# Optimization experiments

Hardware: AMD Instinct MI355X
Metric: run time of the kernel (lower is better)

## Reference

```python
import jax, jax.numpy as jnp
import numpy as np

BITS = 4
GROUP = 128
PACK = 32 // BITS  # 8 values per int32
MASK = (1 << BITS) - 1


def _unpack_weight(qweight, K, N):
    # qweight: [K//PACK, N] int32; PACK 4-bit values packed along K in each int32
    shifts = jnp.arange(PACK, dtype=jnp.int32) * BITS  # [PACK]
    w = (qweight[:, None, :] >> shifts[None, :, None]) & MASK  # [K//PACK, PACK, N]
    return w.reshape(K, N)


def _unpack_zeros(qzeros, G, N):
    # qzeros: [G, N//PACK] int32; PACK 4-bit values packed along N in each int32
    shifts = jnp.arange(PACK, dtype=jnp.int32) * BITS  # [PACK]
    z = (qzeros[:, :, None] >> shifts[None, None, :]) & MASK  # [G, N//PACK, PACK]
    return z.reshape(G, N)


def setup_inputs() -> dict:
    key = jax.random.key(0)
    k1, k2, k3, k4 = jax.random.split(key, 4)
    B, S, K, N = 4, 1024, 4096, 11008
    G = K // GROUP
    x = jax.random.normal(k1, (B, S, K), dtype=jnp.float32)
    qweight = jax.random.randint(k2, (K // PACK, N), 0, 2147483647, dtype=jnp.int32)
    qzeros = jax.random.randint(k3, (G, N // PACK), 0, 2147483647, dtype=jnp.int32)
    scales = jax.random.uniform(k4, (G, N), dtype=jnp.float32) * 0.01
    return {"x": x, "qweight": qweight, "qzeros": qzeros, "scales": scales}


def reference(x, qweight, qzeros, scales):
    K = x.shape[-1]
    G, N = scales.shape
    # dequantize: W[k, n] = (q[k, n] - zero[g(k), n]) * scale[g(k), n]
    w_q = _unpack_weight(qweight, K, N).astype(jnp.float32)   # [K, N]
    zeros = _unpack_zeros(qzeros, G, N).astype(jnp.float32)   # [G, N]
    gid = jnp.arange(K) // GROUP                              # [K]
    W = (w_q - zeros[gid]) * scales[gid]                      # [K, N]
    return jnp.einsum('bsk,kn->bsn', x, W)
```

## Files before the change

### kernel.cpp

```cpp
#include <hip/hip_runtime.h>


#define BK 32
#define LDK 40
#define TILE_BYTES 10240

typedef _Float16 v8h __attribute__((ext_vector_type(8)));
typedef _Float16 half2v __attribute__((ext_vector_type(2)));
typedef float v4f __attribute__((ext_vector_type(4)));

__device__ __forceinline__ unsigned pkrtz_u32(float a, float b) {
  return __builtin_bit_cast(unsigned, __builtin_amdgcn_cvt_pkrtz(a, b));
}

__device__ __forceinline__ void load_lds_16B(const void* g, void* l) {
  __builtin_amdgcn_global_load_lds(
      (const __attribute__((address_space(1))) unsigned*)g,
      (__attribute__((address_space(3))) unsigned*)l, 16, 0, 0);
}

__global__ __launch_bounds__(256)
void prep_x(const float* __restrict__ x, unsigned short* __restrict__ xt, int K) {
  const int kt = blockIdx.x, mt = blockIdx.y;
  const int t = threadIdx.x;
  const int row = t >> 1, half = t & 1;
  const float* src = x + (size_t)(mt * 128 + row) * K + kt * 32 + half * 16;
  const float4 v0 = ((const float4*)src)[0];
  const float4 v1 = ((const float4*)src)[1];
  const float4 v2 = ((const float4*)src)[2];
  const float4 v3 = ((const float4*)src)[3];
  uint4 o0, o1;
  o0.x = pkrtz_u32(v0.x, v0.y); o0.y = pkrtz_u32(v0.z, v0.w);
  o0.z = pkrtz_u32(v1.x, v1.y); o0.w = pkrtz_u32(v1.z, v1.w);
  o1.x = pkrtz_u32(v2.x, v2.y); o1.y = pkrtz_u32(v2.z, v2.w);
  o1.z = pkrtz_u32(v3.x, v3.y); o1.w = pkrtz_u32(v3.z, v3.w);
  unsigned short* dst =
      xt + (size_t)(mt * (K / 32) + kt) * (TILE_BYTES / 2) + row * LDK + half * 16;
  ((uint4*)dst)[0] = o0;
  ((uint4*)(dst + 8))[0] = o1;
}

__global__ __launch_bounds__(512, 4)
void qgemm_dma(const unsigned short* __restrict__ xt,
               const unsigned* __restrict__ qweight,
               const unsigned* __restrict__ qzeros,
               const float* __restrict__ scales,
               float* __restrict__ out,
               int M, int N, int K) {
  __shared__ __align__(16) short As[128][LDK];
  __shared__ __align__(16) short Bs[256][LDK];

  const int tid = threadIdx.x;
  const int lane = tid & 63;
  const int wid = tid >> 6;
  const int n0 = blockIdx.x * 256;
  const int m0 = blockIdx.y * 128;
  const int mt = blockIdx.y;
  const int wm = (wid >> 2) * 64;
  const int wn = (wid & 3) * 64;
  const int lr = lane & 15;
  const int lk = (lane >> 4) * 8;

  const int b_n = tid & 255;
  const int b_kr0 = tid >> 8;
  const int gn = n0 + b_n;
  const unsigned* qwb = qweight + (size_t)b_kr0 * N + gn;

  const char* xt_b = (const char*)xt;
  const int NT = K / BK;

  v4f acc[4][4] = {};

  unsigned b0c, b1c, zpc;
  float scc;
  auto load_b = [&](int t, unsigned& b0, unsigned& b1, unsigned& zp, float& sc) {
    const int kk = t * BK;
    const size_t qoff = (size_t)(kk >> 3) * N;
    b0 = qwb[qoff];
    b1 = qwb[qoff + 2 * (size_t)N];
    const int g = kk >> 7;
    zp = qzeros[(size_t)g * (N >> 3) + (gn >> 3)];
    sc = scales[(size_t)g * N + gn];
  };
  load_b(0, b0c, b1c, zpc, scc);

#pragma unroll 2
  for (int t = 0; t < NT; ++t) {
    {
      const char* g = xt_b + (size_t)(mt * NT + t) * TILE_BYTES +
                      (size_t)wid * 1024 + (size_t)lane * 16;
      char* l = ((char*)&As[0][0]) + wid * 1024;
      load_lds_16B(g, l);
      if (wid < 2) load_lds_16B(g + 8 * 1024, l + 8 * 1024);
    }

    {
      const unsigned z = (zpc >> ((gn & 7) * 4)) & 15u;
      const unsigned hz_u = 0x64006400u | z | (z << 16);
      const half2v hz2 = __builtin_bit_cast(half2v, hz_u);
      const half2v hs2 = __builtin_bit_cast(half2v, pkrtz_u32(scc, scc));
      const unsigned qvs[2] = {b0c, b1c};
#pragma unroll
      for (int q = 0; q < 2; ++q) {
        const int kr = b_kr0 + q * 2;
        const unsigned qv = qvs[q];
        uint4 wv;
        unsigned* wp = (unsigned*)&wv;
#pragma unroll
        for (int j = 0; j < 4; ++j) {
          const unsigned byte = qv >> (8 * j);
          const unsigned pq = 0x64006400u | (byte & 0xFu) | ((byte & 0xF0u) << 12);
          const half2v w2 = (__builtin_bit_cast(half2v, pq) - hz2) * hs2;
          wp[j] = __builtin_bit_cast(unsigned, w2);
        }
        *(uint4*)(&Bs[b_n][kr * 8]) = wv;
      }
    }

    __syncthreads();

    unsigned b0n, b1n, zpn;
    float scn;
    const int tn = (t + 1 < NT) ? (t + 1) : t;
    load_b(tn, b0n, b1n, zpn, scn);

    v8h af[4], bfr[4];
#pragma unroll
    for (int i = 0; i < 4; ++i) {
      af[i] = *(const v8h*)(&As[wm + i * 16 + lr][lk]);
      bfr[i] = *(const v8h*)(&Bs[wn + i * 16 + lr][lk]);
    }
#pragma unroll
    for (int mi = 0; mi < 4; ++mi) {
#pragma unroll
      for (int ni = 0; ni < 4; ++ni) {
        acc[mi][ni] = __builtin_amdgcn_mfma_f32_16x16x32_f16(
            af[mi], bfr[ni], acc[mi][ni], 0, 0, 0);
      }
    }

    __syncthreads();

    b0c = b0n; b1c = b1n; zpc = zpn; scc = scn;
  }

#pragma unroll
  for (int mi = 0; mi < 4; ++mi) {
#pragma unroll
    for (int ni = 0; ni < 4; ++ni) {
#pragma unroll
      for (int r = 0; r < 4; ++r) {
        const int row = m0 + wm + mi * 16 + (lane >> 4) * 4 + r;
        const int col = n0 + wn + ni * 16 + lr;
        out[(size_t)row * N + col] = acc[mi][ni][r];
      }
    }
  }
}

__global__ __launch_bounds__(256, 2)
void qgemm_fused(const float* __restrict__ x,
                 const unsigned* __restrict__ qweight,
                 const unsigned* __restrict__ qzeros,
                 const float* __restrict__ scales,
                 float* __restrict__ out,
                 int M, int N, int K) {
  __shared__ short As[128][LDK];
  __shared__ short Bs[128][LDK];

  const int tid = threadIdx.x;
  const int lane = tid & 63;
  const int wid = tid >> 6;
  const int n0 = blockIdx.x * 128;
  const int m0 = blockIdx.y * 128;
  const int wm = (wid >> 1) * 64;
  const int wn = (wid & 1) * 64;
  const int lr = lane & 15;
  const int lk = (lane >> 4) * 8;

  const int a_row = tid >> 3;
  const int a_col = (tid & 7) * 4;
  const int b_n = tid & 127;
  const int b_kr0 = tid >> 7;
  const int gn = n0 + b_n;

  const float* xb = x + (size_t)(m0 + a_row) * K + a_col;
  const unsigned* qwb = qweight + (size_t)b_kr0 * N + gn;

  v4f acc[4][4] = {};
  const int NT = K / BK;

  float4 axc[4];
  unsigned b0c, b1c, zpc;
  float scc;

  auto load_step = [&](int t, float4 ax[4], unsigned& b0, unsigned& b1,
                       unsigned& zp, float& sc) {
    const int kk = t * BK;
#pragma unroll
    for (int p = 0; p < 4; ++p)
      ax[p] = *(const float4*)(xb + (size_t)(p * 32) * K + kk);
    const size_t qoff = (size_t)(kk >> 3) * N;
    b0 = qwb[qoff];
    b1 = qwb[qoff + 2 * (size_t)N];
    const int g = kk >> 7;
    zp = qzeros[(size_t)g * (N >> 3) + (gn >> 3)];
    sc = scales[(size_t)g * N + gn];
  };

  load_step(0, axc, b0c, b1c, zpc, scc);

#pragma unroll 2
  for (int t = 0; t < NT; ++t) {
    const unsigned z = (zpc >> ((gn & 7) * 4)) & 15u;
    const unsigned hz_u = 0x64006400u | z | (z << 16);
    const half2v hz2 = __builtin_bit_cast(half2v, hz_u);
    const half2v hs2 = __builtin_bit_cast(half2v, pkrtz_u32(scc, scc));

#pragma unroll
    for (int p = 0; p < 4; ++p) {
      const int row = p * 32 + a_row;
      uint2 pv;
      pv.x = pkrtz_u32(axc[p].x, axc[p].y);
      pv.y = pkrtz_u32(axc[p].z, axc[p].w);
      *(uint2*)(&As[row][a_col]) = pv;
    }
    {
      const unsigned qvs[2] = {b0c, b1c};
#pragma unroll
      for (int q = 0; q < 2; ++q) {
        const int kr = b_kr0 + q * 2;
        const unsigned qv = qvs[q];
        uint4 wv;
        unsigned* wp = (unsigned*)&wv;
#pragma unroll
        for (int j = 0; j < 4; ++j) {
          const unsigned byte = qv >> (8 * j);
          const unsigned pq = 0x64006400u | (byte & 0xFu) | ((byte & 0xF0u) << 12);
          const half2v w2 = (__builtin_bit_cast(half2v, pq) - hz2) * hs2;
          wp[j] = __builtin_bit_cast(unsigned, w2);
        }
        *(uint4*)(&Bs[b_n][kr * 8]) = wv;
      }
    }

    __syncthreads();

    float4 axn[4];
    unsigned b0n, b1n, zpn;
    float scn;
    const int tn = (t + 1 < NT) ? (t + 1) : t;
    load_step(tn, axn, b0n, b1n, zpn, scn);

    v8h af[4], bfr[4];
#pragma unroll
    for (int i = 0; i < 4; ++i) {
      af[i] = *(const v8h*)(&As[wm + i * 16 + lr][lk]);
      bfr[i] = *(const v8h*)(&Bs[wn + i * 16 + lr][lk]);
    }
#pragma unroll
    for (int mi = 0; mi < 4; ++mi) {
#pragma unroll
      for (int ni = 0; ni < 4; ++ni) {
        acc[mi][ni] = __builtin_amdgcn_mfma_f32_16x16x32_f16(
            af[mi], bfr[ni], acc[mi][ni], 0, 0, 0);
      }
    }

    __syncthreads();

#pragma unroll
    for (int p = 0; p < 4; ++p) axc[p] = axn[p];
    b0c = b0n; b1c = b1n; zpc = zpn; scc = scn;
  }

#pragma unroll
  for (int mi = 0; mi < 4; ++mi) {
#pragma unroll
    for (int ni = 0; ni < 4; ++ni) {
#pragma unroll
      for (int r = 0; r < 4; ++r) {
        const int row = m0 + wm + mi * 16 + (lane >> 4) * 4 + r;
        const int col = n0 + wn + ni * 16 + lr;
        out[(size_t)row * N + col] = acc[mi][ni][r];
      }
    }
  }
}

extern "C" void kernel_launch(void* const* d_in, const int* in_sizes, int n_in,
                              void* d_out, int out_size, void* d_ws, size_t ws_size,
                              hipStream_t stream) {
  const float* x = (const float*)d_in[0];
  const unsigned* qweight = (const unsigned*)d_in[1];
  const unsigned* qzeros = (const unsigned*)d_in[2];
  const float* scales = (const float*)d_in[3];
  float* out = (float*)d_out;

  const int K = 4096;
  const int N = 11008;
  const int M = in_sizes[0] / K;

  const size_t need = (size_t)(M / 128) * (K / 32) * TILE_BYTES;
  if (ws_size >= need) {
    unsigned short* xt = (unsigned short*)d_ws;
    prep_x<<<dim3(K / 32, M / 128), 256, 0, stream>>>(x, xt, K);
    dim3 grid(N / 256, M / 128);
    qgemm_dma<<<grid, 512, 0, stream>>>(xt, qweight, qzeros, scales, out, M, N, K);
  } else {
    dim3 grid(N / 128, M / 128);
    qgemm_fused<<<grid, 256, 0, stream>>>(x, qweight, qzeros, scales, out, M, N, K);
  }
}
```

Before: 665.9 us.

## Pre-dequantize weights into fp16 tiled workspace and DMA both operands to LDS

Adds a prep_w kernel that dequantizes the 4-bit weights once into an fp16, LDS-ready tiled layout in the workspace. A new qgemm_pre GEMM then streams both A and B tiles with global_load_lds DMA, so the main loop no longer does per-tile unpacking, zero/scale math or register-to-LDS stores. In exchange, dequantization is redone once per forward call and the GEMM reads fp16 weights (about 90MB) instead of packed int4. This path requires a larger workspace and falls back to the old kernels otherwise.

```diff
diff --git a/kernel.cpp b/kernel.cpp
--- a/kernel.cpp
+++ b/kernel.cpp
@@ -4,6 +4,7 @@
 #define BK 32
 #define LDK 40
 #define TILE_BYTES 10240
+#define WTILE_BYTES 20480
 
 typedef _Float16 v8h __attribute__((ext_vector_type(8)));
 typedef _Float16 half2v __attribute__((ext_vector_type(2)));
@@ -40,13 +41,117 @@
   ((uint4*)(dst + 8))[0] = o1;
 }
 
+__global__ __launch_bounds__(256)
+void prep_w(const unsigned* __restrict__ qweight,
+            const unsigned* __restrict__ qzeros,
+            const float* __restrict__ scales,
+            unsigned short* __restrict__ wt, int N, int K) {
+  const int nt = blockIdx.x, kt = blockIdx.y;
+  const int n_loc = threadIdx.x;
+  const int gn = nt * 256 + n_loc;
+  const int g = kt >> 2;
+  const unsigned zp = qzeros[(size_t)g * (N >> 3) + (gn >> 3)];
+  const float s = scales[(size_t)g * N + gn];
+  const unsigned z = (zp >> ((gn & 7) * 4)) & 15u;
+  const unsigned hz_u = 0x64006400u | z | (z << 16);
+  const half2v hz2 = __builtin_bit_cast(half2v, hz_u);
+  const half2v hs2 = __builtin_bit_cast(half2v, pkrtz_u32(s, s));
+  unsigned short* dst =
+      wt + (size_t)(nt * (K / 32) + kt) * (WTILE_BYTES / 2) + n_loc * LDK;
+#pragma unroll
+  for (int kr = 0; kr < 4; ++kr) {
+    const unsigned qv = qweight[(size_t)(kt * 4 + kr) * N + gn];
+    uint4 wv;
+    unsigned* wp = (unsigned*)&wv;
+#pragma unroll
+    for (int j = 0; j < 4; ++j) {
+      const unsigned byte = qv >> (8 * j);
+      const unsigned pq = 0x64006400u | (byte & 0xFu) | ((byte & 0xF0u) << 12);
+      const half2v w2 = (__builtin_bit_cast(half2v, pq) - hz2) * hs2;
+      wp[j] = __builtin_bit_cast(unsigned, w2);
+    }
+    *(uint4*)(dst + kr * 8) = wv;
+  }
+}
+
+__global__ __launch_bounds__(512, 4)
+void qgemm_pre(const unsigned short* __restrict__ xt,
+               const unsigned short* __restrict__ wt,
+               float* __restrict__ out, int M, int N, int K) {
+  __shared__ __align__(16) short As[128][LDK];
+  __shared__ __align__(16) short Bs[256][LDK];
+
+  const int tid = threadIdx.x;
+  const int lane = tid & 63;
+  const int wid = tid >> 6;
+  const int nt = blockIdx.x, mt = blockIdx.y;
+  const int n0 = nt * 256, m0 = mt * 128;
+  const int wm = (wid >> 2) * 64;
+  const int wn = (wid & 3) * 64;
+  const int lr = lane & 15;
+  const int lk = (lane >> 4) * 8;
+
+  const int NT = K / BK;
+  const char* ga = (const char*)xt + (size_t)mt * NT * TILE_BYTES +
+                   wid * 1024 + lane * 16;
+  const char* gb = (const char*)wt + (size_t)nt * NT * WTILE_BYTES +
+                   wid * 1024 + lane * 16;
+  char* la = ((char*)&As[0][0]) + wid * 1024;
+  char* lb = ((char*)&Bs[0][0]) + wid * 1024;
+
+  v4f acc[4][4] = {};
+
+#pragma unroll 2
+  for (int t = 0; t < NT; ++t) {
+    load_lds_16B(ga, la);
+    if (wid < 2) load_lds_16B(ga + 8 * 1024, la + 8 * 1024);
+    load_lds_16B(gb, lb);
+    load_lds_16B(gb + 8 * 1024, lb + 8 * 1024);
+    if (wid < 4) load_lds_16B(gb + 16 * 1024, lb + 16 * 1024);
+
+    __syncthreads();
+
+    v8h af[4], bfr[4];
+#pragma unroll
+    for (int i = 0; i < 4; ++i) {
+      af[i] = *(const v8h*)(&As[wm + i * 16 + lr][lk]);
+      bfr[i] = *(const v8h*)(&Bs[wn + i * 16 + lr][lk]);
+    }
+#pragma unroll
+    for (int mi = 0; mi < 4; ++mi) {
+#pragma unroll
+      for (int ni = 0; ni < 4; ++ni) {
+        acc[mi][ni] = __builtin_amdgcn_mfma_f32_16x16x32_f16(
+            af[mi], bfr[ni], acc[mi][ni], 0, 0, 0);
+      }
+    }
+
+    __syncthreads();
+
+    ga += TILE_BYTES;
+    gb += WTILE_BYTES;
+  }
+
+#pragma unroll
+  for (int mi = 0; mi < 4; ++mi) {
+#pragma unroll
+    for (int ni = 0; ni < 4; ++ni) {
+#pragma unroll
+      for (int r = 0; r < 4; ++r) {
+        const int row = m0 + wm + mi * 16 + (lane >> 4) * 4 + r;
+        const int col = n0 + wn + ni * 16 + lr;
+        out[(size_t)row * N + col] = acc[mi][ni][r];
+      }
+    }
+  }
+}
+
 __global__ __launch_bounds__(512, 4)
 void qgemm_dma(const unsigned short* __restrict__ xt,
                const unsigned* __restrict__ qweight,
                const unsigned* __restrict__ qzeros,
                const float* __restrict__ scales,
-               float* __restrict__ out,
-               int M, int N, int K) {
+               float* __restrict__ out, int M, int N, int K) {
   __shared__ __align__(16) short As[128][LDK];
   __shared__ __align__(16) short Bs[256][LDK];
 
@@ -93,7 +198,6 @@
       load_lds_16B(g, l);
       if (wid < 2) load_lds_16B(g + 8 * 1024, l + 8 * 1024);
     }
-
     {
       const unsigned z = (zpc >> ((gn & 7) * 4)) & 15u;
       const unsigned hz_u = 0x64006400u | z | (z << 16);
@@ -163,8 +267,7 @@
                  const unsigned* __restrict__ qweight,
                  const unsigned* __restrict__ qzeros,
                  const float* __restrict__ scales,
-                 float* __restrict__ out,
-                 int M, int N, int K) {
+                 float* __restrict__ out, int M, int N, int K) {
   __shared__ short As[128][LDK];
   __shared__ short Bs[128][LDK];
 
@@ -301,14 +404,22 @@
   const int N = 11008;
   const int M = in_sizes[0] / K;
 
-  const size_t need = (size_t)(M / 128) * (K / 32) * TILE_BYTES;
-  if (ws_size >= need) {
+  const size_t A_BYTES = (size_t)(M / 128) * (K / 32) * TILE_BYTES;
+  const size_t W_BYTES = (size_t)(N / 256) * (K / 32) * WTILE_BYTES;
+
+  if (ws_size >= A_BYTES + W_BYTES) {
+    unsigned short* xt = (unsigned short*)d_ws;
+    unsigned short* wtp = (unsigned short*)((char*)d_ws + A_BYTES);
+    prep_x<<<dim3(K / 32, M / 128), 256, 0, stream>>>(x, xt, K);
+    prep_w<<<dim3(N / 256, K / 32), 256, 0, stream>>>(qweight, qzeros, scales, wtp, N, K);
+    qgemm_pre<<<dim3(N / 256, M / 128), 512, 0, stream>>>(xt, wtp, out, M, N, K);
+  } else if (ws_size >= A_BYTES) {
     unsigned short* xt = (unsigned short*)d_ws;
     prep_x<<<dim3(K / 32, M / 128), 256, 0, stream>>>(x, xt, K);
-    dim3 grid(N / 256, M / 128);
-    qgemm_dma<<<grid, 512, 0, stream>>>(xt, qweight, qzeros, scales, out, M, N, K);
+    qgemm_dma<<<dim3(N / 256, M / 128), 512, 0, stream>>>(xt, qweight, qzeros, scales,
+                                                          out, M, N, K);
   } else {
-    dim3 grid(N / 128, M / 128);
-    qgemm_fused<<<grid, 256, 0, stream>>>(x, qweight, qzeros, scales, out, M, N, K);
-  }
-}
+    qgemm_fused<<<dim3(N / 128, M / 128), 256, 0, stream>>>(x, qweight, qzeros, scales,
+                                                            out, M, N, K);
+  }
+}
```

Result: slower. 720.9 us (+8.3%).
